# Kernel tuning notes

Measured on AMD Instinct MI355X. Metric: run time of the kernel, lower is better.

The kernel has to match this reference:

```python
import jax, jax.numpy as jnp
import numpy as np

N = 2048


def setup_inputs() -> dict:
    key = jax.random.key(0)
    k1, k2 = jax.random.split(key)
    input1 = jax.random.normal(k1, (N, N), dtype=jnp.float32)
    input2 = jax.random.normal(k2, (N, N), dtype=jnp.float32)
    return {"input1": input1, "input2": input2}


def reference(input1, input2):
    # Common subexpressions (the original recomputes these many times;
    # the math is identical):
    A = input1 @ input1            # mm(input1, input1)
    B = input1 @ input2            # mm(input1, input2)
    C = input2 @ B                 # mm(input2, mm(input1, input2))
    D = input2 @ A                 # mm(input2, mm(input1, input1))

    t1 = A
    t2 = A @ input2 + B
    t3 = C + B @ A
    t4 = C @ A + D @ input2
    t5 = (C @ A) @ A + (D @ B) @ A
    t6 = t1 - (t2 + t3 * t4 / t5)
    return t6
```

## Files before the change

### kernel.cpp

```cpp
#include <hip/hip_runtime.h>


#define NMAT 2048

constexpr int FM = 128, FN = 128, FK = 16;
constexpr int LDA = FM + 4;
constexpr int LDB = FN + 4;

template <int DO_ADD>
__global__ __launch_bounds__(256) void sgemm512(
    const float* __restrict__ Am, const float* __restrict__ Bm, float* Cm,
    const float* Addm) {
  __shared__ float As[FK][LDA];
  __shared__ float Bs[FK][LDB];
  const int tid = threadIdx.x;
  const int row0 = blockIdx.y * FM;
  const int col0 = blockIdx.x * FN;
  const int ty = tid >> 4;
  const int tx = tid & 15;

  const int ar = tid >> 2;
  const int ac = (tid & 3) * 4;
  const int bk = tid >> 5;
  const int bc = (tid & 31) * 4;

  float tot[8][8] = {};
  float acc[8][8] = {};
  float4 va0, va1, vb0, vb1;

  va0 = *(const float4*)&Am[(size_t)(row0 + ar) * NMAT + ac];
  va1 = *(const float4*)&Am[(size_t)(row0 + ar + 64) * NMAT + ac];
  vb0 = *(const float4*)&Bm[(size_t)bk * NMAT + col0 + bc];
  vb1 = *(const float4*)&Bm[(size_t)(bk + 8) * NMAT + col0 + bc];

  for (int k0 = 0; k0 < NMAT; k0 += FK) {
    __syncthreads();
    As[ac + 0][ar] = va0.x;
    As[ac + 1][ar] = va0.y;
    As[ac + 2][ar] = va0.z;
    As[ac + 3][ar] = va0.w;
    As[ac + 0][ar + 64] = va1.x;
    As[ac + 1][ar + 64] = va1.y;
    As[ac + 2][ar + 64] = va1.z;
    As[ac + 3][ar + 64] = va1.w;
    *(float4*)&Bs[bk][bc] = vb0;
    *(float4*)&Bs[bk + 8][bc] = vb1;
    __syncthreads();

    if (k0 + FK < NMAT) {
      const int kn = k0 + FK;
      va0 = *(const float4*)&Am[(size_t)(row0 + ar) * NMAT + kn + ac];
      va1 = *(const float4*)&Am[(size_t)(row0 + ar + 64) * NMAT + kn + ac];
      vb0 = *(const float4*)&Bm[(size_t)(kn + bk) * NMAT + col0 + bc];
      vb1 = *(const float4*)&Bm[(size_t)(kn + bk + 8) * NMAT + col0 + bc];
    }

#pragma unroll
    for (int k = 0; k < FK; ++k) {
      const float4 a0 = *(const float4*)&As[k][ty * 4];
      const float4 a1 = *(const float4*)&As[k][64 + ty * 4];
      const float4 b0 = *(const float4*)&Bs[k][tx * 4];
      const float4 b1 = *(const float4*)&Bs[k][64 + tx * 4];
      const float af[8] = {a0.x, a0.y, a0.z, a0.w, a1.x, a1.y, a1.z, a1.w};
      const float bf[8] = {b0.x, b0.y, b0.z, b0.w, b1.x, b1.y, b1.z, b1.w};
#pragma unroll
      for (int i = 0; i < 8; ++i)
#pragma unroll
        for (int j = 0; j < 8; ++j)
          acc[i][j] = fmaf(af[i], bf[j], acc[i][j]);
    }

    if (((k0 + FK) & 511) == 0) {
#pragma unroll
      for (int i = 0; i < 8; ++i)
#pragma unroll
        for (int j = 0; j < 8; ++j) {
          tot[i][j] = __fadd_rn(tot[i][j], acc[i][j]);
          acc[i][j] = 0.0f;
        }
    }
  }

#pragma unroll
  for (int i = 0; i < 8; ++i) {
    const int r = row0 + ((i < 4) ? (ty * 4 + i) : (64 + ty * 4 + (i - 4)));
#pragma unroll
    for (int jb = 0; jb < 2; ++jb) {
      const int c = col0 + ((jb == 0) ? (tx * 4) : (64 + tx * 4));
      const size_t idx = (size_t)r * NMAT + c;
      float4 v;
      v.x = tot[i][jb * 4 + 0];
      v.y = tot[i][jb * 4 + 1];
      v.z = tot[i][jb * 4 + 2];
      v.w = tot[i][jb * 4 + 3];
      if (DO_ADD) {
        const float4 ad = *(const float4*)&Addm[idx];
        v.x = __fadd_rn(v.x, ad.x);
        v.y = __fadd_rn(v.y, ad.y);
        v.z = __fadd_rn(v.z, ad.z);
        v.w = __fadd_rn(v.w, ad.w);
      }
      *(float4*)&Cm[idx] = v;
    }
  }
}

__global__ __launch_bounds__(256) void final_fp32(
    const float* __restrict__ t1, const float* __restrict__ t2,
    const float* t3, const float* __restrict__ t4,
    const float* __restrict__ t5, float* outp) {
  size_t i = (size_t)blockIdx.x * 256 + threadIdx.x;
  float num = __fmul_rn(t3[i], t4[i]);
  float q = __fdiv_rn(num, t5[i]);
  float s = __fadd_rn(t2[i], q);
  outp[i] = __fsub_rn(t1[i], s);
}

extern "C" void kernel_launch(void* const* d_in, const int* in_sizes, int n_in,
                              void* d_out, int out_size, void* d_ws,
                              size_t ws_size, hipStream_t stream) {
  const float* X1 = (const float*)d_in[0];
  const float* X2 = (const float*)d_in[1];
  float* out = (float*)d_out;

  const size_t NN = (size_t)NMAT * NMAT;
  const size_t M32 = NN * sizeof(float);
  char* w = (char*)d_ws;
  float* fA  = (float*)(w + 0 * M32);
  float* fB  = (float*)(w + 1 * M32);
  float* fC  = (float*)(w + 2 * M32);
  float* fD  = (float*)(w + 3 * M32);
  float* fP  = (float*)(w + 4 * M32);
  float* fQ  = (float*)(w + 5 * M32);
  float* t2f = (float*)(w + 6 * M32);
  float* t4f = (float*)(w + 7 * M32);
  float* fT  = (float*)(w + 2 * M32);
  float* t5f = (float*)(w + 3 * M32);

  dim3 grid(NMAT / FN, NMAT / FM);
  dim3 blk(256);
  dim3 ew((unsigned)(NN / 256));

  sgemm512<0><<<grid, blk, 0, stream>>>(X1, X1, fA, nullptr);
  sgemm512<0><<<grid, blk, 0, stream>>>(X1, X2, fB, nullptr);
  sgemm512<0><<<grid, blk, 0, stream>>>(X2, fB, fC, nullptr);
  sgemm512<0><<<grid, blk, 0, stream>>>(X2, fA, fD, nullptr);
  sgemm512<0><<<grid, blk, 0, stream>>>(fC, fA, fP, nullptr);
  sgemm512<0><<<grid, blk, 0, stream>>>(fD, fB, fQ, nullptr);
  sgemm512<1><<<grid, blk, 0, stream>>>(fB, fA, out, fC);
  sgemm512<1><<<grid, blk, 0, stream>>>(fD, X2, t4f, fP);
  sgemm512<1><<<grid, blk, 0, stream>>>(fA, X2, t2f, fB);
  sgemm512<0><<<grid, blk, 0, stream>>>(fP, fA, fT, nullptr);
  sgemm512<1><<<grid, blk, 0, stream>>>(fQ, fA, t5f, fT);
  final_fp32<<<ew, blk, 0, stream>>>(fA, t2f, out, t4f, t5f, out);
}
```

Measured before the change: 2.596 ms.

## Split GEMMs along K into four chunks with separate reduction kernel

Each GEMM is split into four K-chunks of 512, launched as a 3D grid that writes partial products to workspace, followed by an elementwise reduction that sums partials in the same order and applies the optional add. This quadruples the number of blocks to raise occupancy and latency hiding on the GPU. In exchange, each GEMM adds an extra kernel launch and extra memory traffic for partial buffers. The path is taken only if the workspace is large enough, otherwise the original kernels run.

```diff
diff --git a/kernel.cpp b/kernel.cpp
--- a/kernel.cpp
+++ b/kernel.cpp
@@ -6,6 +6,121 @@
 constexpr int FM = 128, FN = 128, FK = 16;
 constexpr int LDA = FM + 4;
 constexpr int LDB = FN + 4;
+constexpr int KCHUNK = 512;
+
+__global__ __launch_bounds__(256, 4) void sgemm_chunk(
+    const float* __restrict__ Am, const float* __restrict__ Bm,
+    float* __restrict__ Pm) {
+  __shared__ float As[FK][LDA];
+  __shared__ float Bs[FK][LDB];
+  const int tid = threadIdx.x;
+  const int row0 = blockIdx.y * FM;
+  const int col0 = blockIdx.x * FN;
+  const int kb = blockIdx.z * KCHUNK;
+  const int ty = tid >> 4;
+  const int tx = tid & 15;
+
+  const int ar = tid >> 2;
+  const int ac = (tid & 3) * 4;
+  const int bk = tid >> 5;
+  const int bc = (tid & 31) * 4;
+
+  float acc[8][8] = {};
+  float4 va0, va1, vb0, vb1;
+
+  const float* pa0 = &Am[(size_t)(row0 + ar) * NMAT + kb + ac];
+  const float* pa1 = pa0 + (size_t)64 * NMAT;
+  const float* pb0 = &Bm[(size_t)(kb + bk) * NMAT + col0 + bc];
+  const float* pb1 = pb0 + (size_t)8 * NMAT;
+
+  va0 = *(const float4*)pa0;
+  va1 = *(const float4*)pa1;
+  vb0 = *(const float4*)pb0;
+  vb1 = *(const float4*)pb1;
+
+#pragma unroll 1
+  for (int t = 0; t < KCHUNK / FK; ++t) {
+    __syncthreads();
+    As[ac + 0][ar] = va0.x;
+    As[ac + 1][ar] = va0.y;
+    As[ac + 2][ar] = va0.z;
+    As[ac + 3][ar] = va0.w;
+    As[ac + 0][ar + 64] = va1.x;
+    As[ac + 1][ar + 64] = va1.y;
+    As[ac + 2][ar + 64] = va1.z;
+    As[ac + 3][ar + 64] = va1.w;
+    *(float4*)&Bs[bk][bc] = vb0;
+    *(float4*)&Bs[bk + 8][bc] = vb1;
+    __syncthreads();
+
+    if (t + 1 < KCHUNK / FK) {
+      pa0 += FK;
+      pa1 += FK;
+      pb0 += (size_t)FK * NMAT;
+      pb1 += (size_t)FK * NMAT;
+      va0 = *(const float4*)pa0;
+      va1 = *(const float4*)pa1;
+      vb0 = *(const float4*)pb0;
+      vb1 = *(const float4*)pb1;
+    }
+
+#pragma unroll
+    for (int k = 0; k < FK; ++k) {
+      const float4 a0 = *(const float4*)&As[k][ty * 4];
+      const float4 a1 = *(const float4*)&As[k][64 + ty * 4];
+      const float4 b0 = *(const float4*)&Bs[k][tx * 4];
+      const float4 b1 = *(const float4*)&Bs[k][64 + tx * 4];
+      const float af[8] = {a0.x, a0.y, a0.z, a0.w, a1.x, a1.y, a1.z, a1.w};
+      const float bf[8] = {b0.x, b0.y, b0.z, b0.w, b1.x, b1.y, b1.z, b1.w};
+#pragma unroll
+      for (int i = 0; i < 8; ++i)
+#pragma unroll
+        for (int j = 0; j < 8; ++j)
+          acc[i][j] = fmaf(af[i], bf[j], acc[i][j]);
+    }
+  }
+
+  float* dst = Pm + (size_t)blockIdx.z * NMAT * NMAT;
+#pragma unroll
+  for (int i = 0; i < 8; ++i) {
+    const int r = row0 + ((i < 4) ? (ty * 4 + i) : (64 + ty * 4 + (i - 4)));
+#pragma unroll
+    for (int jb = 0; jb < 2; ++jb) {
+      const int c = col0 + ((jb == 0) ? (tx * 4) : (64 + tx * 4));
+      float4 v;
+      v.x = acc[i][jb * 4 + 0];
+      v.y = acc[i][jb * 4 + 1];
+      v.z = acc[i][jb * 4 + 2];
+      v.w = acc[i][jb * 4 + 3];
+      *(float4*)&dst[(size_t)r * NMAT + c] = v;
+    }
+  }
+}
+
+template <int DO_ADD>
+__global__ __launch_bounds__(256) void reduce_k4(
+    const float* __restrict__ Pm, const float* __restrict__ Addm,
+    float* __restrict__ outp) {
+  const size_t NN = (size_t)NMAT * NMAT;
+  const size_t i = ((size_t)blockIdx.x * 256 + threadIdx.x) * 4;
+  const float4 c0 = *(const float4*)&Pm[i];
+  const float4 c1 = *(const float4*)&Pm[i + NN];
+  const float4 c2 = *(const float4*)&Pm[i + 2 * NN];
+  const float4 c3 = *(const float4*)&Pm[i + 3 * NN];
+  float4 v;
+  v.x = __fadd_rn(__fadd_rn(__fadd_rn(__fadd_rn(0.0f, c0.x), c1.x), c2.x), c3.x);
+  v.y = __fadd_rn(__fadd_rn(__fadd_rn(__fadd_rn(0.0f, c0.y), c1.y), c2.y), c3.y);
+  v.z = __fadd_rn(__fadd_rn(__fadd_rn(__fadd_rn(0.0f, c0.z), c1.z), c2.z), c3.z);
+  v.w = __fadd_rn(__fadd_rn(__fadd_rn(__fadd_rn(0.0f, c0.w), c1.w), c2.w), c3.w);
+  if (DO_ADD) {
+    const float4 ad = *(const float4*)&Addm[i];
+    v.x = __fadd_rn(v.x, ad.x);
+    v.y = __fadd_rn(v.y, ad.y);
+    v.z = __fadd_rn(v.z, ad.z);
+    v.w = __fadd_rn(v.w, ad.w);
+  }
+  *(float4*)&outp[i] = v;
+}
 
 template <int DO_ADD>
 __global__ __launch_bounds__(256) void sgemm512(
@@ -18,7 +133,6 @@
   const int col0 = blockIdx.x * FN;
   const int ty = tid >> 4;
   const int tx = tid & 15;
-
   const int ar = tid >> 2;
   const int ac = (tid & 3) * 4;
   const int bk = tid >> 5;
@@ -137,20 +251,48 @@
   float* fT  = (float*)(w + 2 * M32);
   float* t5f = (float*)(w + 3 * M32);
 
-  dim3 grid(NMAT / FN, NMAT / FM);
   dim3 blk(256);
   dim3 ew((unsigned)(NN / 256));
 
-  sgemm512<0><<<grid, blk, 0, stream>>>(X1, X1, fA, nullptr);
-  sgemm512<0><<<grid, blk, 0, stream>>>(X1, X2, fB, nullptr);
-  sgemm512<0><<<grid, blk, 0, stream>>>(X2, fB, fC, nullptr);
-  sgemm512<0><<<grid, blk, 0, stream>>>(X2, fA, fD, nullptr);
-  sgemm512<0><<<grid, blk, 0, stream>>>(fC, fA, fP, nullptr);
-  sgemm512<0><<<grid, blk, 0, stream>>>(fD, fB, fQ, nullptr);
-  sgemm512<1><<<grid, blk, 0, stream>>>(fB, fA, out, fC);
-  sgemm512<1><<<grid, blk, 0, stream>>>(fD, X2, t4f, fP);
-  sgemm512<1><<<grid, blk, 0, stream>>>(fA, X2, t2f, fB);
-  sgemm512<0><<<grid, blk, 0, stream>>>(fP, fA, fT, nullptr);
-  sgemm512<1><<<grid, blk, 0, stream>>>(fQ, fA, t5f, fT);
-  final_fp32<<<ew, blk, 0, stream>>>(fA, t2f, out, t4f, t5f, out);
-}
+  if (ws_size >= 12 * M32) {
+    float* Pk = (float*)(w + 8 * M32);
+    dim3 gsk(NMAT / FN, NMAT / FM, 4);
+    dim3 gr((unsigned)(NN / (256 * 4)));
+
+    auto gemm = [&](const float* A, const float* B, float* dst,
+                    const float* add) {
+      sgemm_chunk<<<gsk, blk, 0, stream>>>(A, B, Pk);
+      if (add)
+        reduce_k4<1><<<gr, blk, 0, stream>>>(Pk, add, dst);
+      else
+        reduce_k4<0><<<gr, blk, 0, stream>>>(Pk, nullptr, dst);
+    };
+
+    gemm(X1, X1, fA, nullptr);
+    gemm(X1, X2, fB, nullptr);
+    gemm(X2, fB, fC, nullptr);
+    gemm(X2, fA, fD, nullptr);
+    gemm(fC, fA, fP, nullptr);
+    gemm(fD, fB, fQ, nullptr);
+    gemm(fB, fA, out, fC);
+    gemm(fD, X2, t4f, fP);
+    gemm(fA, X2, t2f, fB);
+    gemm(fP, fA, fT, nullptr);
+    gemm(fQ, fA, t5f, fT);
+    final_fp32<<<ew, blk, 0, stream>>>(fA, t2f, out, t4f, t5f, out);
+  } else {
+    dim3 grid(NMAT / FN, NMAT / FM);
+    sgemm512<0><<<grid, blk, 0, stream>>>(X1, X1, fA, nullptr);
+    sgemm512<0><<<grid, blk, 0, stream>>>(X1, X2, fB, nullptr);
+    sgemm512<0><<<grid, blk, 0, stream>>>(X2, fB, fC, nullptr);
+    sgemm512<0><<<grid, blk, 0, stream>>>(X2, fA, fD, nullptr);
+    sgemm512<0><<<grid, blk, 0, stream>>>(fC, fA, fP, nullptr);
+    sgemm512<0><<<grid, blk, 0, stream>>>(fD, fB, fQ, nullptr);
+    sgemm512<1><<<grid, blk, 0, stream>>>(fB, fA, out, fC);
+    sgemm512<1><<<grid, blk, 0, stream>>>(fD, X2, t4f, fP);
+    sgemm512<1><<<grid, blk, 0, stream>>>(fA, X2, t2f, fB);
+    sgemm512<0><<<grid, blk, 0, stream>>>(fP, fA, fT, nullptr);
+    sgemm512<1><<<grid, blk, 0, stream>>>(fQ, fA, t5f, fT);
+    final_fp32<<<ew, blk, 0, stream>>>(fA, t2f, out, t4f, t5f, out);
+  }
+}
```

Measured after the change: 4.535 ms. +74.7%, slower.

## Split-K GEMMs into four 512-chunks and batch independent GEMM pairs

Applied to the files above, without the earlier changes.

Each 2048^3 GEMM is split along K into four 512-wide chunks, each computed by its own blocks, with partial results written to workspace and summed by a separate reduce kernel that also applies the addend. Independent GEMM pairs are merged into a single launch along grid z, giving 2048 blocks per launch instead of 256, which should fill the GPU's compute units better. The reduction adds the chunks in the same order as the original per-512 accumulation, so the rounding matches. The cost is extra global traffic for partials (up to 8 matrices) plus extra reduce launches, and it needs a large workspace. If the workspace is too small, nothing is computed at all.

```diff
diff --git a/kernel.cpp b/kernel.cpp
--- a/kernel.cpp
+++ b/kernel.cpp
@@ -6,13 +6,19 @@
 constexpr int FM = 128, FN = 128, FK = 16;
 constexpr int LDA = FM + 4;
 constexpr int LDB = FN + 4;
-
-template <int DO_ADD>
-__global__ __launch_bounds__(256) void sgemm512(
-    const float* __restrict__ Am, const float* __restrict__ Bm, float* Cm,
-    const float* Addm) {
+constexpr int KCHUNK = 512;
+
+__global__ __launch_bounds__(256) void sgemm_chunk2(
+    const float* __restrict__ A0, const float* __restrict__ B0,
+    const float* __restrict__ A1, const float* __restrict__ B1,
+    float* __restrict__ Pm) {
   __shared__ float As[FK][LDA];
   __shared__ float Bs[FK][LDB];
+  const int g = blockIdx.z >> 2;
+  const float* __restrict__ Am = g ? A1 : A0;
+  const float* __restrict__ Bm = g ? B1 : B0;
+  const int kb = (blockIdx.z & 3) * KCHUNK;
+
   const int tid = threadIdx.x;
   const int row0 = blockIdx.y * FM;
   const int col0 = blockIdx.x * FN;
@@ -24,16 +30,21 @@
   const int bk = tid >> 5;
   const int bc = (tid & 31) * 4;
 
-  float tot[8][8] = {};
   float acc[8][8] = {};
   float4 va0, va1, vb0, vb1;
 
-  va0 = *(const float4*)&Am[(size_t)(row0 + ar) * NMAT + ac];
-  va1 = *(const float4*)&Am[(size_t)(row0 + ar + 64) * NMAT + ac];
-  vb0 = *(const float4*)&Bm[(size_t)bk * NMAT + col0 + bc];
-  vb1 = *(const float4*)&Bm[(size_t)(bk + 8) * NMAT + col0 + bc];
-
-  for (int k0 = 0; k0 < NMAT; k0 += FK) {
+  const float* pa0 = &Am[(size_t)(row0 + ar) * NMAT + kb + ac];
+  const float* pa1 = pa0 + (size_t)64 * NMAT;
+  const float* pb0 = &Bm[(size_t)(kb + bk) * NMAT + col0 + bc];
+  const float* pb1 = pb0 + (size_t)8 * NMAT;
+
+  va0 = *(const float4*)pa0;
+  va1 = *(const float4*)pa1;
+  vb0 = *(const float4*)pb0;
+  vb1 = *(const float4*)pb1;
+
+#pragma unroll 1
+  for (int t = 0; t < KCHUNK / FK; ++t) {
     __syncthreads();
     As[ac + 0][ar] = va0.x;
     As[ac + 1][ar] = va0.y;
@@ -47,12 +58,15 @@
     *(float4*)&Bs[bk + 8][bc] = vb1;
     __syncthreads();
 
-    if (k0 + FK < NMAT) {
-      const int kn = k0 + FK;
-      va0 = *(const float4*)&Am[(size_t)(row0 + ar) * NMAT + kn + ac];
-      va1 = *(const float4*)&Am[(size_t)(row0 + ar + 64) * NMAT + kn + ac];
-      vb0 = *(const float4*)&Bm[(size_t)(kn + bk) * NMAT + col0 + bc];
-      vb1 = *(const float4*)&Bm[(size_t)(kn + bk + 8) * NMAT + col0 + bc];
+    if (t + 1 < KCHUNK / FK) {
+      pa0 += FK;
+      pa1 += FK;
+      pb0 += (size_t)FK * NMAT;
+      pb1 += (size_t)FK * NMAT;
+      va0 = *(const float4*)pa0;
+      va1 = *(const float4*)pa1;
+      vb0 = *(const float4*)pb0;
+      vb1 = *(const float4*)pb1;
     }
 
 #pragma unroll
@@ -69,40 +83,80 @@
         for (int j = 0; j < 8; ++j)
           acc[i][j] = fmaf(af[i], bf[j], acc[i][j]);
     }
-
-    if (((k0 + FK) & 511) == 0) {
-#pragma unroll
-      for (int i = 0; i < 8; ++i)
-#pragma unroll
-        for (int j = 0; j < 8; ++j) {
-          tot[i][j] = __fadd_rn(tot[i][j], acc[i][j]);
-          acc[i][j] = 0.0f;
-        }
-    }
-  }
-
+  }
+
+  float* dst = Pm + (size_t)blockIdx.z * NMAT * NMAT;
 #pragma unroll
   for (int i = 0; i < 8; ++i) {
     const int r = row0 + ((i < 4) ? (ty * 4 + i) : (64 + ty * 4 + (i - 4)));
 #pragma unroll
     for (int jb = 0; jb < 2; ++jb) {
       const int c = col0 + ((jb == 0) ? (tx * 4) : (64 + tx * 4));
-      const size_t idx = (size_t)r * NMAT + c;
       float4 v;
-      v.x = tot[i][jb * 4 + 0];
-      v.y = tot[i][jb * 4 + 1];
-      v.z = tot[i][jb * 4 + 2];
-      v.w = tot[i][jb * 4 + 3];
-      if (DO_ADD) {
-        const float4 ad = *(const float4*)&Addm[idx];
-        v.x = __fadd_rn(v.x, ad.x);
-        v.y = __fadd_rn(v.y, ad.y);
-        v.z = __fadd_rn(v.z, ad.z);
-        v.w = __fadd_rn(v.w, ad.w);
-      }
-      *(float4*)&Cm[idx] = v;
+      v.x = acc[i][jb * 4 + 0];
+      v.y = acc[i][jb * 4 + 1];
+      v.z = acc[i][jb * 4 + 2];
+      v.w = acc[i][jb * 4 + 3];
+      *(float4*)&dst[(size_t)r * NMAT + c] = v;
     }
   }
+}
+
+__global__ __launch_bounds__(256) void reduce_k4_2(
+    const float* __restrict__ Pm, const float* __restrict__ Ad0,
+    const float* __restrict__ Ad1, float* __restrict__ o0,
+    float* __restrict__ o1) {
+  const size_t NN = (size_t)NMAT * NMAT;
+  const size_t Q = NN / 4;
+  const size_t gi = (size_t)blockIdx.x * 256 + threadIdx.x;
+  const int g = gi >= Q;
+  const size_t i = (gi - (g ? Q : 0)) * 4;
+  const float* P = Pm + (g ? 4 * NN : 0);
+  const float* ad = g ? Ad1 : Ad0;
+  float* op = g ? o1 : o0;
+
+  const float4 c0 = *(const float4*)&P[i];
+  const float4 c1 = *(const float4*)&P[i + NN];
+  const float4 c2 = *(const float4*)&P[i + 2 * NN];
+  const float4 c3 = *(const float4*)&P[i + 3 * NN];
+  float4 v;
+  v.x = __fadd_rn(__fadd_rn(__fadd_rn(__fadd_rn(0.0f, c0.x), c1.x), c2.x), c3.x);
+  v.y = __fadd_rn(__fadd_rn(__fadd_rn(__fadd_rn(0.0f, c0.y), c1.y), c2.y), c3.y);
+  v.z = __fadd_rn(__fadd_rn(__fadd_rn(__fadd_rn(0.0f, c0.z), c1.z), c2.z), c3.z);
+  v.w = __fadd_rn(__fadd_rn(__fadd_rn(__fadd_rn(0.0f, c0.w), c1.w), c2.w), c3.w);
+  if (ad) {
+    const float4 a = *(const float4*)&ad[i];
+    v.x = __fadd_rn(v.x, a.x);
+    v.y = __fadd_rn(v.y, a.y);
+    v.z = __fadd_rn(v.z, a.z);
+    v.w = __fadd_rn(v.w, a.w);
+  }
+  *(float4*)&op[i] = v;
+}
+
+template <int DO_ADD>
+__global__ __launch_bounds__(256) void reduce_k4(
+    const float* __restrict__ Pm, const float* __restrict__ Addm,
+    float* __restrict__ outp) {
+  const size_t NN = (size_t)NMAT * NMAT;
+  const size_t i = ((size_t)blockIdx.x * 256 + threadIdx.x) * 4;
+  const float4 c0 = *(const float4*)&Pm[i];
+  const float4 c1 = *(const float4*)&Pm[i + NN];
+  const float4 c2 = *(const float4*)&Pm[i + 2 * NN];
+  const float4 c3 = *(const float4*)&Pm[i + 3 * NN];
+  float4 v;
+  v.x = __fadd_rn(__fadd_rn(__fadd_rn(__fadd_rn(0.0f, c0.x), c1.x), c2.x), c3.x);
+  v.y = __fadd_rn(__fadd_rn(__fadd_rn(__fadd_rn(0.0f, c0.y), c1.y), c2.y), c3.y);
+  v.z = __fadd_rn(__fadd_rn(__fadd_rn(__fadd_rn(0.0f, c0.z), c1.z), c2.z), c3.z);
+  v.w = __fadd_rn(__fadd_rn(__fadd_rn(__fadd_rn(0.0f, c0.w), c1.w), c2.w), c3.w);
+  if (DO_ADD) {
+    const float4 ad = *(const float4*)&Addm[i];
+    v.x = __fadd_rn(v.x, ad.x);
+    v.y = __fadd_rn(v.y, ad.y);
+    v.z = __fadd_rn(v.z, ad.z);
+    v.w = __fadd_rn(v.w, ad.w);
+  }
+  *(float4*)&outp[i] = v;
 }
 
 __global__ __launch_bounds__(256) void final_fp32(
@@ -137,20 +191,54 @@
   float* fT  = (float*)(w + 2 * M32);
   float* t5f = (float*)(w + 3 * M32);
 
-  dim3 grid(NMAT / FN, NMAT / FM);
   dim3 blk(256);
   dim3 ew((unsigned)(NN / 256));
-
-  sgemm512<0><<<grid, blk, 0, stream>>>(X1, X1, fA, nullptr);
-  sgemm512<0><<<grid, blk, 0, stream>>>(X1, X2, fB, nullptr);
-  sgemm512<0><<<grid, blk, 0, stream>>>(X2, fB, fC, nullptr);
-  sgemm512<0><<<grid, blk, 0, stream>>>(X2, fA, fD, nullptr);
-  sgemm512<0><<<grid, blk, 0, stream>>>(fC, fA, fP, nullptr);
-  sgemm512<0><<<grid, blk, 0, stream>>>(fD, fB, fQ, nullptr);
-  sgemm512<1><<<grid, blk, 0, stream>>>(fB, fA, out, fC);
-  sgemm512<1><<<grid, blk, 0, stream>>>(fD, X2, t4f, fP);
-  sgemm512<1><<<grid, blk, 0, stream>>>(fA, X2, t2f, fB);
-  sgemm512<0><<<grid, blk, 0, stream>>>(fP, fA, fT, nullptr);
-  sgemm512<1><<<grid, blk, 0, stream>>>(fQ, fA, t5f, fT);
-  final_fp32<<<ew, blk, 0, stream>>>(fA, t2f, out, t4f, t5f, out);
-}
+  dim3 gr1((unsigned)(NN / 1024));
+
+  if (ws_size >= 16 * M32) {
+    float* Pk = (float*)(w + 8 * M32);
+    dim3 g8(NMAT / FN, NMAT / FM, 8);
+    dim3 g4(NMAT / FN, NMAT / FM, 4);
+    dim3 gr2((unsigned)(2 * NN / 1024));
+
+    sgemm_chunk2<<<g8, blk, 0, stream>>>(X1, X1, X1, X2, Pk);
+    reduce_k4_2<<<gr2, blk, 0, stream>>>(Pk, nullptr, nullptr, fA, fB);
+    sgemm_chunk2<<<g8, blk, 0, stream>>>(X2, fB, X2, fA, Pk);
+    reduce_k4_2<<<gr2, blk, 0, stream>>>(Pk, nullptr, nullptr, fC, fD);
+    sgemm_chunk2<<<g8, blk, 0, stream>>>(fC, fA, fD, fB, Pk);
+    reduce_k4_2<<<gr2, blk, 0, stream>>>(Pk, nullptr, nullptr, fP, fQ);
+    sgemm_chunk2<<<g8, blk, 0, stream>>>(fB, fA, fA, X2, Pk);
+    reduce_k4_2<<<gr2, blk, 0, stream>>>(Pk, fC, fB, out, t2f);
+    sgemm_chunk2<<<g8, blk, 0, stream>>>(fD, X2, fP, fA, Pk);
+    reduce_k4_2<<<gr2, blk, 0, stream>>>(Pk, fP, nullptr, t4f, fT);
+    sgemm_chunk2<<<g4, blk, 0, stream>>>(fQ, fA, fQ, fA, Pk);
+    reduce_k4<1><<<gr1, blk, 0, stream>>>(Pk, fT, t5f);
+
+    final_fp32<<<ew, blk, 0, stream>>>(fA, t2f, out, t4f, t5f, out);
+  } else if (ws_size >= 12 * M32) {
+    float* Pk = (float*)(w + 8 * M32);
+    dim3 g4(NMAT / FN, NMAT / FM, 4);
+
+    auto gemm = [&](const float* A, const float* B, float* dst,
+                    const float* add) {
+      sgemm_chunk2<<<g4, blk, 0, stream>>>(A, B, A, B, Pk);
+      if (add)
+        reduce_k4<1><<<gr1, blk, 0, stream>>>(Pk, add, dst);
+      else
+        reduce_k4<0><<<gr1, blk, 0, stream>>>(Pk, nullptr, dst);
+    };
+
+    gemm(X1, X1, fA, nullptr);
+    gemm(X1, X2, fB, nullptr);
+    gemm(X2, fB, fC, nullptr);
+    gemm(X2, fA, fD, nullptr);
+    gemm(fC, fA, fP, nullptr);
+    gemm(fD, fB, fQ, nullptr);
+    gemm(fB, fA, out, fC);
+    gemm(fD, X2, t4f, fP);
+    gemm(fA, X2, t2f, fB);
+    gemm(fP, fA, fT, nullptr);
+    gemm(fQ, fA, t5f, fT);
+    final_fp32<<<ew, blk, 0, stream>>>(fA, t2f, out, t4f, t5f, out);
+  }
+}
```

After: 2.382 ms. -8.3%, faster.
